# Kernel tuning notes

Measured on AMD Instinct MI355X. Metric: run time of the kernel, lower is better.

Reference implementation:

```python
import jax, jax.numpy as jnp
import numpy as np

B, T, C = 8, 2048, 1024
HEAD = 64

def setup_inputs() -> dict:
    key = jax.random.key(0)
    k1, k2 = jax.random.split(key)
    x = jax.random.normal(k1, (B, T, C), dtype=jnp.float32)
    # nn.Linear(dim_embedding, head_size, bias=False) weight: [head_size, dim_embedding]
    W_k = jax.random.normal(k2, (HEAD, C), dtype=jnp.float32) * (C ** -0.5)
    return {"x": x, "W_k": W_k}

def reference(x, W_k):
    # Faithful to source: q, k, v are ALL computed with the `key` projection,
    # and the scale is C**-0.5 (embedding dim), as written in the torch code.
    Bx, Tx, Cx = x.shape
    k = jnp.einsum('btc,hc->bth', x, W_k)   # [B,T,HEAD]
    q = k
    v = k
    scale = Cx ** -0.5
    weight = jnp.einsum('bth,bsh->bts', q, k) * scale  # [B,T,T]
    causal = jnp.tril(jnp.ones((Tx, Tx), dtype=bool))
    weight = jnp.where(causal, weight, -jnp.inf)
    weight = jax.nn.softmax(weight, axis=-1)
    # dropout: eval-mode identity (p=0.2 at train time in the source)
    out = jnp.einsum('bts,bsh->bth', weight, v)  # [B,T,HEAD]
    return out
```

## Files before the change

kernel.cpp:

```cpp
#include <hip/hip_runtime.h>
#include <hip/hip_bf16.h>
#include <math.h>

#define SEQ   2048
#define CDIM  1024
#define HD    64
#define NROW  16384
#define CEXP 0.04508422002778112f

typedef float  f32x4  __attribute__((ext_vector_type(4)));
typedef __bf16 bf16x8 __attribute__((ext_vector_type(8)));
typedef int    i32x4  __attribute__((ext_vector_type(4)));

#define AS1 __attribute__((address_space(1)))
#define AS3 __attribute__((address_space(3)))

static __device__ __forceinline__ unsigned pk2(float a, float b) {
    unsigned ua = __builtin_bit_cast(unsigned, a);
    unsigned ub = __builtin_bit_cast(unsigned, b);
    ua += 0x7fffu + ((ua >> 16) & 1u);
    ub += 0x7fffu + ((ub >> 16) & 1u);
    return (ua >> 16) | (ub & 0xffff0000u);
}

static __device__ __forceinline__ bf16x8 cvt8(f32x4 lo, f32x4 hi) {
    i32x4 w = { (int)pk2(lo[0], lo[1]), (int)pk2(lo[2], lo[3]),
                (int)pk2(hi[0], hi[1]), (int)pk2(hi[2], hi[3]) };
    return __builtin_bit_cast(bf16x8, w);
}

template<int S>
struct XProl {
    static __device__ __forceinline__ void run(f32x4 (&XA)[8], f32x4 (&XB)[8],
                                               unsigned long long xa) {
        constexpr int OFF = S * 128;
        asm volatile("global_load_dwordx4 %0, %2, off offset:%3\n\t"
                     "global_load_dwordx4 %1, %2, off offset:%4"
                     : "=&v"(XA[S]), "=&v"(XB[S])
                     : "v"(xa), "n"(OFF), "n"(OFF + 16)
                     : "memory");
        if constexpr (S + 1 < 8) XProl<S + 1>::run(XA, XB, xa);
    }
};

template<int T>
struct XLoop {
    static __device__ __forceinline__ void run(f32x4 (&XA)[8], f32x4 (&XB)[8],
                                               unsigned long long xa,
                                               const char* const (&wp)[4][2],
                                               f32x4 (&acc)[4]) {
        constexpr int WT = (T < 24) ? 14 : 2 * (31 - T);
        asm volatile("s_waitcnt vmcnt(%0)" :: "n"(WT) : "memory");
        __builtin_amdgcn_sched_barrier(0);
        bf16x8 A = cvt8(XA[T & 7], XB[T & 7]);
        #pragma unroll
        for (int nt = 0; nt < 4; ++nt) {
            bf16x8 B = *(const bf16x8*)(wp[nt][T & 1] + (T >> 1) * 128);
            acc[nt] = __builtin_amdgcn_mfma_f32_16x16x32_bf16(A, B, acc[nt], 0, 0, 0);
        }
        if constexpr (T < 24) {
            constexpr int OFF = (T + 8) * 128;
            asm volatile("global_load_dwordx4 %0, %2, off offset:%3\n\t"
                         "global_load_dwordx4 %1, %2, off offset:%4"
                         : "=&v"(XA[T & 7]), "=&v"(XB[T & 7])
                         : "v"(xa), "n"(OFF), "n"(OFF + 16)
                         : "memory");
        }
        if constexpr (T + 1 < 32) XLoop<T + 1>::run(XA, XB, xa, wp, acc);
    }
};

__global__ __launch_bounds__(256, 1) void proj_kernel(const float* __restrict__ x,
                                                      const float* __restrict__ W,
                                                      unsigned short* __restrict__ Ko,
                                                      uint2* __restrict__ KV2) {
    __shared__ __align__(16) char wlds[131072];
    __shared__ __align__(16) unsigned short tb[4][16][64];

    const int tid = threadIdx.x;
    const int wid = tid >> 6, l = tid & 63, lm = l & 15, lg = l >> 4;
    const int bid = blockIdx.x;

    #pragma unroll
    for (int c = 0; c < 4; ++c) {
        float4 wv[16];
        #pragma unroll
        for (int j = 0; j < 16; ++j)
            wv[j] = *(const float4*)(W + ((size_t)(c * 16 + j) * 256 + tid) * 4);
        #pragma unroll
        for (int j = 0; j < 16; ++j) {
            const int r = c * 16 + j;
            uint2 p = make_uint2(pk2(wv[j].x, wv[j].y), pk2(wv[j].z, wv[j].w));
            *(uint2*)(wlds + r * 2048 + ((tid * 8) ^ ((r & 7) << 4))) = p;
        }
    }

    const int row = bid * 64 + wid * 16 + lm;
    unsigned long long xa =
        (unsigned long long)(const void*)(x + (size_t)row * CDIM + lg * 8);
    f32x4 XA[8], XB[8];
    XProl<0>::run(XA, XB, xa);

    asm volatile("s_waitcnt lgkmcnt(0)" ::: "memory");
    __builtin_amdgcn_sched_barrier(0);
    __builtin_amdgcn_s_barrier();
    __builtin_amdgcn_sched_barrier(0);

    const int hb = (lm >> 2) & 1;
    const int L  = ((lg ^ (lm & 3)) << 4);
    const char* wp[4][2];
    #pragma unroll
    for (int nt = 0; nt < 4; ++nt) {
        const char* base = wlds + (nt * 16 + lm) * 2048;
        wp[nt][0] = base + hb * 64 + L;
        wp[nt][1] = base + (1 - hb) * 64 + L;
    }

    f32x4 acc[4];
    acc[0] = acc[1] = acc[2] = acc[3] = (f32x4){0.f, 0.f, 0.f, 0.f};
    XLoop<0>::run(XA, XB, xa, wp, acc);

    #pragma unroll
    for (int nt = 0; nt < 4; ++nt)
        #pragma unroll
        for (int r = 0; r < 4; ++r)
            tb[wid][lg * 4 + r][nt * 16 + lm] =
                (unsigned short)(pk2(acc[nt][r], 0.f) & 0xffffu);
    const size_t m0r = (size_t)bid * 64 + wid * 16;
    {
        const char* tbase = (const char*)&tb[wid][0][0];
        i32x4 v0 = *(const i32x4*)(tbase + l * 16);
        i32x4 v1 = *(const i32x4*)(tbase + 1024 + l * 16);
        char* kbase = (char*)(Ko + m0r * HD);
        *(i32x4*)(kbase + l * 16)        = v0;
        *(i32x4*)(kbase + 1024 + l * 16) = v1;
    }
    const size_t g = (size_t)bid * 4 + wid;
    #pragma unroll
    for (int nt = 0; nt < 4; ++nt)
        KV2[(g * 4 + nt) * 64 + l] =
            make_uint2(pk2(acc[nt][0], acc[nt][1]), pk2(acc[nt][2], acc[nt][3]));
}

struct KT { bf16x8 ka0, ka1; uint2 bv[4]; };

static __device__ __forceinline__ KT load_tile(const unsigned short* __restrict__ Kb,
                                               const uint2* __restrict__ KVb,
                                               int kt, int lm, int lg, int l) {
    KT t;
    const unsigned short* ar = Kb + (size_t)(kt * 16 + lm) * HD + lg * 8;
    t.ka0 = *(const bf16x8*)ar;
    t.ka1 = *(const bf16x8*)(ar + 32);
    const uint2* vp = KVb + (size_t)kt * 256 + l;
    #pragma unroll
    for (int nt = 0; nt < 4; ++nt) t.bv[nt] = vp[nt * 64];
    return t;
}

static __device__ __forceinline__ void proc_tile(const KT& t, bf16x8 bq0, bf16x8 bq1,
                                                 bool diag, int lm, int lg,
                                                 float& ls, f32x4 o[4]) {
    f32x4 s4 = (f32x4){0.f, 0.f, 0.f, 0.f};
    s4 = __builtin_amdgcn_mfma_f32_16x16x32_bf16(t.ka0, bq0, s4, 0, 0, 0);
    s4 = __builtin_amdgcn_mfma_f32_16x16x32_bf16(t.ka1, bq1, s4, 0, 0, 0);
    float s0 = s4[0], s1 = s4[1], s2 = s4[2], s3 = s4[3];
    if (diag) {
        const int kb = lg * 4;
        s0 = (kb + 0 > lm) ? -1e30f : s0;
        s1 = (kb + 1 > lm) ? -1e30f : s1;
        s2 = (kb + 2 > lm) ? -1e30f : s2;
        s3 = (kb + 3 > lm) ? -1e30f : s3;
    }
    float p0 = __builtin_amdgcn_exp2f(s0 * CEXP);
    float p1 = __builtin_amdgcn_exp2f(s1 * CEXP);
    float p2 = __builtin_amdgcn_exp2f(s2 * CEXP);
    float p3 = __builtin_amdgcn_exp2f(s3 * CEXP);
    ls += (p0 + p1) + (p2 + p3);
    i32x4 pw = { (int)pk2(p0, p1), (int)pk2(p2, p3), 0, 0 };
    bf16x8 pa = __builtin_bit_cast(bf16x8, pw);
    #pragma unroll
    for (int nt = 0; nt < 4; ++nt) {
        i32x4 vw = { (int)t.bv[nt].x, (int)t.bv[nt].y, 0, 0 };
        bf16x8 bvx = __builtin_bit_cast(bf16x8, vw);
        o[nt] = __builtin_amdgcn_mfma_f32_16x16x32_bf16(pa, bvx, o[nt], 0, 0, 0);
    }
}

__global__ __launch_bounds__(256, 1) void attn_kernel(const unsigned short* __restrict__ K,
                                                      const uint2* __restrict__ KV2,
                                                      float* __restrict__ out) {
    __shared__ float oS[4][4][16][68];
    __shared__ float lS[4][4][16];
    const int tid = threadIdx.x;
    const int wid = tid >> 6, l = tid & 63, lm = l & 15, lg = l >> 4;
    const int b = blockIdx.x >> 5, j = blockIdx.x & 31;
    const int qts[4] = { 2 * j, 2 * j + 1, 126 - 2 * j, 127 - 2 * j };
    const unsigned short* Kb  = K   + (size_t)b * SEQ * HD;
    const uint2*          KVb = KV2 + (size_t)b * 128 * 256;

    bf16x8 bq0[4], bq1[4];
    #pragma unroll
    for (int s = 0; s < 4; ++s) {
        const unsigned short* qr = Kb + (size_t)(qts[s] * 16 + lm) * HD + lg * 8;
        bq0[s] = *(const bf16x8*)qr;
        bq1[s] = *(const bf16x8*)(qr + 32);
    }

    float ls[4] = { 0.f, 0.f, 0.f, 0.f };
    f32x4 o[4][4];
    #pragma unroll
    for (int s = 0; s < 4; ++s)
        #pragma unroll
        for (int nt = 0; nt < 4; ++nt) o[s][nt] = (f32x4){0.f, 0.f, 0.f, 0.f};

    auto process = [&](const KT& t, int kt) {
        #pragma unroll
        for (int s = 0; s < 4; ++s)
            if (kt <= qts[s])
                proc_tile(t, bq0[s], bq1[s], kt == qts[s], lm, lg, ls[s], o[s]);
    };

    const int qmax = qts[3];
    KT A = load_tile(Kb, KVb, wid, lm, lg, l);
    int kt = wid;
    while (kt + 4 <= qmax) {
        KT B = load_tile(Kb, KVb, kt + 4, lm, lg, l);
        process(A, kt);
        A = B; kt += 4;
    }
    process(A, kt);

    #pragma unroll
    for (int s = 0; s < 4; ++s) {
        float lsum = ls[s];
        lsum += __shfl_xor(lsum, 16);
        lsum += __shfl_xor(lsum, 32);
        #pragma unroll
        for (int nt = 0; nt < 4; ++nt)
            #pragma unroll
            for (int r = 0; r < 4; ++r)
                oS[s][wid][lg * 4 + r][nt * 16 + lm] = o[s][nt][r];
        if (lg == 0) lS[s][wid][lm] = lsum;
    }
    __syncthreads();

    const int slot = wid;
    const int row  = l >> 2;
    const int cg   = l & 3;
    const int qt   = (slot < 2) ? (2 * j + slot) : (126 - 2 * j + (slot - 2));
    float Lsum = lS[slot][0][row] + lS[slot][1][row] + lS[slot][2][row] + lS[slot][3][row];
    const float inv = 1.f / Lsum;
    float* op = out + ((size_t)b * SEQ + qt * 16 + row) * HD + cg * 16;
    #pragma unroll
    for (int q4 = 0; q4 < 4; ++q4) {
        f32x4 a = (f32x4){0.f, 0.f, 0.f, 0.f};
        #pragma unroll
        for (int w = 0; w < 4; ++w)
            a += *(const f32x4*)&oS[slot][w][row][cg * 16 + q4 * 4];
        *(f32x4*)(op + q4 * 4) = a * inv;
    }
}

extern "C" void kernel_launch(void* const* d_in, const int* in_sizes, int n_in,
                              void* d_out, int out_size, void* d_ws, size_t ws_size,
                              hipStream_t stream) {
    const float* x  = (const float*)d_in[0];
    const float* Wk = (const float*)d_in[1];
    float* o        = (float*)d_out;
    unsigned short* Kp = (unsigned short*)d_ws;
    uint2* KV2 = (uint2*)(Kp + (size_t)NROW * HD);

    proj_kernel<<<256, 256, 0, stream>>>(x, Wk, Kp, KV2);
    attn_kernel<<<256, 256, 0, stream>>>(Kp, KV2, o);
}
```

Measured before the change: 38.74 us.

## Pre-convert W to bf16 fragments and stream x through double-buffered LDS

A new small kernel converts W_k to bf16 once, in MFMA-fragment order. The projection kernel now loads those W fragments straight from global memory into registers, double-buffered across K steps. Before, every block re-converted the whole weight into 128KB of LDS. The x tile is now staged into a 64KB double-buffered LDS region with global_load_lds, and the vmcnt waits are hand-tuned. Less LDS lets two blocks share a CU, but the extra kernel launch and more register pressure from the W buffers could offset the gain.

```diff
diff --git a/kernel.cpp b/kernel.cpp
--- a/kernel.cpp
+++ b/kernel.cpp
@@ -14,6 +14,8 @@
 
 #define AS1 __attribute__((address_space(1)))
 #define AS3 __attribute__((address_space(3)))
+#define VWC(N) asm volatile("s_waitcnt vmcnt(" #N ")" ::: "memory")
+#define SB0()  __builtin_amdgcn_sched_barrier(0)
 
 static __device__ __forceinline__ unsigned pk2(float a, float b) {
     unsigned ua = __builtin_bit_cast(unsigned, a);
@@ -29,96 +31,118 @@
     return __builtin_bit_cast(bf16x8, w);
 }
 
-template<int S>
-struct XProl {
-    static __device__ __forceinline__ void run(f32x4 (&XA)[8], f32x4 (&XB)[8],
-                                               unsigned long long xa) {
-        constexpr int OFF = S * 128;
-        asm volatile("global_load_dwordx4 %0, %2, off offset:%3\n\t"
-                     "global_load_dwordx4 %1, %2, off offset:%4"
-                     : "=&v"(XA[S]), "=&v"(XB[S])
-                     : "v"(xa), "n"(OFF), "n"(OFF + 16)
+__global__ __launch_bounds__(256) void wconv_kernel(const float* __restrict__ W,
+                                                    uint2* __restrict__ Wf) {
+    const int f = blockIdx.x * 256 + threadIdx.x;
+    const int lane = f & 63, nt = (f >> 6) & 3, ks = f >> 8;
+    const int head = nt * 16 + (lane & 15);
+    const int k0 = ks * 32 + (lane >> 4) * 8;
+    const float* src = W + (size_t)head * CDIM + k0;
+    float4 a = *(const float4*)src;
+    float4 b = *(const float4*)(src + 4);
+    Wf[f * 2]     = make_uint2(pk2(a.x, a.y), pk2(a.z, a.w));
+    Wf[f * 2 + 1] = make_uint2(pk2(b.x, b.y), pk2(b.z, b.w));
+}
+
+template<int T, int I = 0>
+struct BPre {
+    static __device__ __forceinline__ void run(f32x4 (&BB)[16], unsigned long long wb) {
+        constexpr int j2 = I >> 2, nt = I & 3;
+        asm volatile("global_load_dwordx4 %0, %1, off offset:%2"
+                     : "=&v"(BB[I])
+                     : "v"(wb + (unsigned long long)((T * 4 + j2) * 4096)), "n"(nt * 1024)
                      : "memory");
-        if constexpr (S + 1 < 8) XProl<S + 1>::run(XA, XB, xa);
+        if constexpr (I + 1 < 16) BPre<T, I + 1>::run(BB, wb);
     }
 };
 
-template<int T>
-struct XLoop {
-    static __device__ __forceinline__ void run(f32x4 (&XA)[8], f32x4 (&XB)[8],
-                                               unsigned long long xa,
-                                               const char* const (&wp)[4][2],
-                                               f32x4 (&acc)[4]) {
-        constexpr int WT = (T < 24) ? 14 : 2 * (31 - T);
-        asm volatile("s_waitcnt vmcnt(%0)" :: "n"(WT) : "memory");
-        __builtin_amdgcn_sched_barrier(0);
-        bf16x8 A = cvt8(XA[T & 7], XB[T & 7]);
-        #pragma unroll
-        for (int nt = 0; nt < 4; ++nt) {
-            bf16x8 B = *(const bf16x8*)(wp[nt][T & 1] + (T >> 1) * 128);
-            acc[nt] = __builtin_amdgcn_mfma_f32_16x16x32_bf16(A, B, acc[nt], 0, 0, 0);
+template<int T, class F>
+struct Step {
+    static __device__ __forceinline__ void run(f32x4 (&Bev)[16], f32x4 (&Bod)[16],
+                                               unsigned long long wb, const char* xbF,
+                                               int wid, int lm, int lg,
+                                               f32x4 (&acc)[4], F& stage) {
+        constexpr int bs = T & 1;
+        f32x4 (&BC)[16] = bs ? Bod : Bev;
+        f32x4 (&BN)[16] = bs ? Bev : Bod;
+        const char* ab = xbF + bs * 32768 + (wid * 16 + lm) * 512;
+        const int asw = (lm & 7) << 4;
+
+        auto dot = [&](int j) {
+            f32x4 alo = *(const f32x4*)(ab + ((j * 128 + lg * 32) ^ asw));
+            f32x4 ahi = *(const f32x4*)(ab + ((j * 128 + lg * 32 + 16) ^ asw));
+            bf16x8 A = cvt8(alo, ahi);
+            #pragma unroll
+            for (int nt = 0; nt < 4; ++nt)
+                acc[nt] = __builtin_amdgcn_mfma_f32_16x16x32_bf16(
+                    A, __builtin_bit_cast(bf16x8, BC[j * 4 + nt]), acc[nt], 0, 0, 0);
+        };
+
+        if constexpr (T < 7) { VWC(20); } else { VWC(12); }
+        SB0();
+        dot(0);
+        if constexpr (T < 7) { VWC(16); } else { VWC(8); }
+        SB0();
+        dot(1);
+        if constexpr (T + 1 <= 7) {
+            SB0();
+            BPre<T + 1>::run(BN, wb);
+            SB0();
         }
-        if constexpr (T < 24) {
-            constexpr int OFF = (T + 8) * 128;
-            asm volatile("global_load_dwordx4 %0, %2, off offset:%3\n\t"
-                         "global_load_dwordx4 %1, %2, off offset:%4"
-                         : "=&v"(XA[T & 7]), "=&v"(XB[T & 7])
-                         : "v"(xa), "n"(OFF), "n"(OFF + 16)
-                         : "memory");
+        if constexpr (T < 7) { VWC(28); } else { VWC(4); }
+        SB0();
+        dot(2);
+        if constexpr (T < 7) { VWC(24); } else { VWC(0); }
+        SB0();
+        dot(3);
+        if constexpr (T + 2 <= 7) {
+            SB0();
+            stage(T + 2, (T + 2) & 1);
+            SB0();
         }
-        if constexpr (T + 1 < 32) XLoop<T + 1>::run(XA, XB, xa, wp, acc);
+        if constexpr (T + 1 <= 7)
+            Step<T + 1, F>::run(Bev, Bod, wb, xbF, wid, lm, lg, acc, stage);
     }
 };
 
-__global__ __launch_bounds__(256, 1) void proj_kernel(const float* __restrict__ x,
-                                                      const float* __restrict__ W,
+__global__ __launch_bounds__(256, 2) void proj_kernel(const float* __restrict__ x,
+                                                      const uint2* __restrict__ Wf,
                                                       unsigned short* __restrict__ Ko,
                                                       uint2* __restrict__ KV2) {
-    __shared__ __align__(16) char wlds[131072];
+    __shared__ __align__(16) char xb[65536];
     __shared__ __align__(16) unsigned short tb[4][16][64];
 
     const int tid = threadIdx.x;
     const int wid = tid >> 6, l = tid & 63, lm = l & 15, lg = l >> 4;
     const int bid = blockIdx.x;
 
-    #pragma unroll
-    for (int c = 0; c < 4; ++c) {
-        float4 wv[16];
-        #pragma unroll
-        for (int j = 0; j < 16; ++j)
-            wv[j] = *(const float4*)(W + ((size_t)(c * 16 + j) * 256 + tid) * 4);
-        #pragma unroll
-        for (int j = 0; j < 16; ++j) {
-            const int r = c * 16 + j;
-            uint2 p = make_uint2(pk2(wv[j].x, wv[j].y), pk2(wv[j].z, wv[j].w));
-            *(uint2*)(wlds + r * 2048 + ((tid * 8) ^ ((r & 7) << 4))) = p;
+    auto stage = [&](int t, int bs) {
+        #pragma unroll
+        for (int i = 0; i < 8; ++i) {
+            const int r2 = wid * 16 + 2 * i;
+            const int rl = r2 + (l >> 5);
+            const int colb = ((l & 31) * 16) ^ ((rl & 7) << 4);
+            const float* src = x + (size_t)(bid * 64 + rl) * CDIM + t * 128 + (colb >> 2);
+            __builtin_amdgcn_global_load_lds((const AS1 void*)src,
+                (AS3 void*)(xb + bs * 32768 + r2 * 512), 16, 0, 0);
         }
-    }
-
-    const int row = bid * 64 + wid * 16 + lm;
-    unsigned long long xa =
-        (unsigned long long)(const void*)(x + (size_t)row * CDIM + lg * 8);
-    f32x4 XA[8], XB[8];
-    XProl<0>::run(XA, XB, xa);
-
-    asm volatile("s_waitcnt lgkmcnt(0)" ::: "memory");
-    __builtin_amdgcn_sched_barrier(0);
-    __builtin_amdgcn_s_barrier();
-    __builtin_amdgcn_sched_barrier(0);
-
-    const int hb = (lm >> 2) & 1;
-    const int L  = ((lg ^ (lm & 3)) << 4);
-    const char* wp[4][2];
-    #pragma unroll
-    for (int nt = 0; nt < 4; ++nt) {
-        const char* base = wlds + (nt * 16 + lm) * 2048;
-        wp[nt][0] = base + hb * 64 + L;
-        wp[nt][1] = base + (1 - hb) * 64 + L;
-    }
-
+    };
+
+    const unsigned long long wb =
+        (unsigned long long)(const void*)Wf + (unsigned)(l * 16);
+    f32x4 Bev[16], Bod[16];
     f32x4 acc[4];
     acc[0] = acc[1] = acc[2] = acc[3] = (f32x4){0.f, 0.f, 0.f, 0.f};
-    XLoop<0>::run(XA, XB, xa, wp, acc);
+
+    SB0();
+    stage(0, 0);
+    SB0();
+    BPre<0>::run(Bev, wb);
+    SB0();
+    stage(1, 1);
+    SB0();
+
+    Step<0, decltype(stage)>::run(Bev, Bod, wb, xb, wid, lm, lg, acc, stage);
 
     #pragma unroll
     for (int nt = 0; nt < 4; ++nt)
@@ -269,7 +293,9 @@
     float* o        = (float*)d_out;
     unsigned short* Kp = (unsigned short*)d_ws;
     uint2* KV2 = (uint2*)(Kp + (size_t)NROW * HD);
-
-    proj_kernel<<<256, 256, 0, stream>>>(x, Wk, Kp, KV2);
+    uint2* Wf  = KV2 + (size_t)1024 * 256;
+
+    wconv_kernel<<<32, 256, 0, stream>>>(Wk, Wf);
+    proj_kernel<<<256, 256, 0, stream>>>(x, Wf, Kp, KV2);
     attn_kernel<<<256, 256, 0, stream>>>(Kp, KV2, o);
 }
```

Measured after the change: 41.18 us. +6.3%, slower.
